# Kernel tuning notes

Hardware: AMD Instinct MI355X
Metric: run time of the kernel (lower is better)

## Reference

```python
import jax, jax.numpy as jnp
import numpy as np

B, T, S = 16, 512, 512
V, E, H = 10000, 512, 1024
L, K, MAXLEN = 6, 3, 1024
PAD_VAL = 1.0  # torch code pads conv input with tgt_pad_idx as a float value


def setup_inputs() -> dict:
    key = jax.random.key(0)
    ks = jax.random.split(key, 12)
    g = lambda k, shape: (jax.random.normal(k, shape, jnp.float32) * 0.02)
    return {
        "tgt": jax.random.randint(ks[0], (B, T), 0, V),
        "encoder_conved": jax.random.normal(ks[1], (B, S, E), jnp.float32),
        "encoder_combined": jax.random.normal(ks[2], (B, S, E), jnp.float32),
        "tok_emb": g(ks[3], (V, E)),
        "pos_emb": g(ks[4], (MAXLEN, E)),
        "emb2hid_w": g(ks[5], (E, H)), "emb2hid_b": jnp.zeros((H,), jnp.float32),
        "hid2emb_w": g(ks[6], (H, E)), "hid2emb_b": jnp.zeros((E,), jnp.float32),
        "attn_hid2emb_w": g(ks[7], (H, E)), "attn_hid2emb_b": jnp.zeros((E,), jnp.float32),
        "attn_emb2hid_w": g(ks[8], (E, H)), "attn_emb2hid_b": jnp.zeros((H,), jnp.float32),
        "fc_out_w": g(ks[9], (E, V)), "fc_out_b": jnp.zeros((V,), jnp.float32),
        "conv_w": g(ks[10], (L, 2 * H, H, K)),  # torch Conv1d weight: [out, in, k]
        "conv_b": jnp.zeros((L, 2 * H), jnp.float32),
    }


def reference(tgt, encoder_conved, encoder_combined, tok_emb, pos_emb,
              emb2hid_w, emb2hid_b, hid2emb_w, hid2emb_b,
              attn_hid2emb_w, attn_hid2emb_b, attn_emb2hid_w, attn_emb2hid_b,
              fc_out_w, fc_out_b, conv_w, conv_b):
    scale = jnp.float32(np.sqrt(0.5))
    b, t = tgt.shape
    h = emb2hid_w.shape[1]
    k = conv_w.shape[-1]

    # embeddings (dropout=0 -> identity)
    embedded = tok_emb[tgt] + pos_emb[jnp.arange(t)][None, :, :]   # [B,T,E]
    conv_input = (embedded @ emb2hid_w + emb2hid_b).transpose(0, 2, 1)  # [B,H,T]

    attention = None
    for l in range(conv_w.shape[0]):
        # causal left-pad with the (float) pad-index value, as in the torch code
        pad = jnp.full((b, h, k - 1), PAD_VAL, conv_input.dtype)
        x = jnp.concatenate([pad, conv_input], axis=2)              # [B,H,T+K-1]
        conved = jax.lax.conv_general_dilated(
            x, conv_w[l], window_strides=(1,), padding='VALID',
            dimension_numbers=('NCH', 'OIH', 'NCH')) + conv_b[l][None, :, None]  # [B,2H,T]
        a, g = jnp.split(conved, 2, axis=1)
        conved = a * jax.nn.sigmoid(g)                              # GLU -> [B,H,T]

        # single-head attention over encoder states
        conved_emb = conved.transpose(0, 2, 1) @ attn_hid2emb_w + attn_hid2emb_b  # [B,T,E]
        combined = (conved_emb + embedded) * scale
        energy = jnp.einsum('bte,bse->bts', combined, encoder_conved)
        attention = jax.nn.softmax(energy, axis=2)                  # [B,T,S]
        attended = jnp.einsum('bts,bse->bte', attention, encoder_combined)
        attended = attended @ attn_emb2hid_w + attn_emb2hid_b       # [B,T,H]
        conved = (conved + attended.transpose(0, 2, 1)) * scale     # [B,H,T]

        conv_input = (conved + conv_input) * scale                  # scaled residual

    conved = conv_input.transpose(0, 2, 1) @ hid2emb_w + hid2emb_b  # [B,T,E]
    output = conved @ fc_out_w + fc_out_b                           # [B,T,V]
    return output, attention
```

## Files before the change

### kernel.cpp

```cpp
#include <hip/hip_runtime.h>
#include <hip/hip_bf16.h>

typedef __attribute__((ext_vector_type(4))) float f32x4;
typedef __attribute__((ext_vector_type(8))) short short8;

#define DEVFN __device__ __forceinline__

static constexpr int Bn = 16, Tn = 512, Sn = 512, Vn = 10000, En = 512, Hn = 1024, Ln = 6;
static constexpr int Mn = Bn * Tn;
static constexpr float kScale = 0.70710678118654752440f;

DEVFN float bf2f(__hip_bfloat16 x) { return __bfloat162float(x); }
DEVFN __hip_bfloat16 f2bf(float x) { return __float2bfloat16(x); }

struct bf16x4 { __hip_bfloat16 x, y, z, w; };

DEVFN void gload_lds16(const short* g, short* l) {
    __builtin_amdgcn_global_load_lds((const __attribute__((address_space(1))) void*)g,
                                     (__attribute__((address_space(3))) void*)l, 16, 0, 0);
}


__global__ void padfill_kernel(__hip_bfloat16* p) {
    p[threadIdx.x] = f2bf(1.0f);
}

__global__ void embed_kernel(const int* __restrict__ tgt, const float* __restrict__ tok,
                             const float* __restrict__ pos, const float* __restrict__ bah,
                             __hip_bfloat16* __restrict__ out, __hip_bfloat16* __restrict__ outA) {
    int row = blockIdx.x;
    int t = row & (Tn - 1);
    int v = tgt[row];
    const float* tr = tok + (long)v * En;
    const float* pr = pos + (long)t * En;
    int e = threadIdx.x * 4;
    float4 a = *(const float4*)(tr + e);
    float4 b = *(const float4*)(pr + e);
    float4 bb = *(const float4*)(bah + e);
    bf16x4 o{f2bf(a.x + b.x), f2bf(a.y + b.y), f2bf(a.z + b.z), f2bf(a.w + b.w)};
    *(bf16x4*)(out + (long)row * En + e) = o;
    bf16x4 oa{f2bf(kScale * (a.x + b.x + bb.x)), f2bf(kScale * (a.y + b.y + bb.y)),
              f2bf(kScale * (a.z + b.z + bb.z)), f2bf(kScale * (a.w + b.w + bb.w))};
    *(bf16x4*)(outA + (long)row * En + e) = oa;
}

__global__ void transpose_f32_bf16(const float* __restrict__ src, __hip_bfloat16* __restrict__ dst,
                                   int R, int C, long sZi, long sZo) {
    __shared__ float tile[32][33];
    src += (long)blockIdx.z * sZi;
    dst += (long)blockIdx.z * sZo;
    int c0 = blockIdx.x * 32, r0 = blockIdx.y * 32;
    for (int i = threadIdx.y; i < 32; i += 8) {
        int r = r0 + i, c = c0 + threadIdx.x;
        tile[i][threadIdx.x] = (r < R && c < C) ? src[(long)r * C + c] : 0.f;
    }
    __syncthreads();
    for (int i = threadIdx.y; i < 32; i += 8) {
        int c = c0 + i, r = r0 + threadIdx.x;
        if (c < C && r < R) dst[(long)c * R + r] = f2bf(tile[threadIdx.x][i]);
    }
}

__global__ void convert_bf16_kernel(const float* __restrict__ src, __hip_bfloat16* __restrict__ dst,
                                    long n4) {
    long i = (long)blockIdx.x * blockDim.x + threadIdx.x;
    if (i >= n4) return;
    long j = i * 4;
    float4 v = *(const float4*)(src + j);
    bf16x4 o{f2bf(v.x), f2bf(v.y), f2bf(v.z), f2bf(v.w)};
    *(bf16x4*)(dst + j) = o;
}

__global__ __launch_bounds__(256) void wpack2_kernel(const float* __restrict__ convw,
                                                     __hip_bfloat16* __restrict__ wp, int l) {
    __shared__ float row[3 * Hn];
    int c = blockIdx.x;
    int grp = c >> 5, w = c & 31;
    int o = (w < 16) ? grp * 16 + w : Hn + grp * 16 + (w - 16);
    const float* src = convw + ((long)(l * 2 * Hn + o)) * (Hn * 3);
#pragma unroll
    for (int j = 0; j < 3; ++j) {
        int idx = (j * 256 + threadIdx.x) * 4;
        *(float4*)&row[idx] = *(const float4*)(src + idx);
    }
    __syncthreads();
    __hip_bfloat16* dst = wp + (long)c * (3 * Hn);
#pragma unroll
    for (int j = 0; j < 3; ++j) {
        int kk = (j * 256 + threadIdx.x) * 4;
        int tap = kk >> 10;
        int i = kk & (Hn - 1);
        bf16x4 v{f2bf(row[i * 3 + tap]), f2bf(row[(i + 1) * 3 + tap]),
                 f2bf(row[(i + 2) * 3 + tap]), f2bf(row[(i + 3) * 3 + tap])};
        *(bf16x4*)(dst + kk) = v;
    }
}

__global__ __launch_bounds__(256) void softmax_kernel(const float* __restrict__ energy,
                                                      float* __restrict__ attn_f32,
                                                      __hip_bfloat16* __restrict__ attn_bf) {
    int row = blockIdx.x;
    const float* e = energy + (long)row * Sn;
    int tid = threadIdx.x;
    float v0 = e[tid], v1 = e[tid + 256];
    float m = fmaxf(v0, v1);
    for (int off = 32; off; off >>= 1) m = fmaxf(m, __shfl_xor(m, off));
    __shared__ float redm[4];
    __shared__ float reds[4];
    int lane = tid & 63, w = tid >> 6;
    if (lane == 0) redm[w] = m;
    __syncthreads();
    m = fmaxf(fmaxf(redm[0], redm[1]), fmaxf(redm[2], redm[3]));
    float x0 = __expf(v0 - m), x1 = __expf(v1 - m);
    float s = x0 + x1;
    for (int off = 32; off; off >>= 1) s += __shfl_xor(s, off);
    if (lane == 0) reds[w] = s;
    __syncthreads();
    s = reds[0] + reds[1] + reds[2] + reds[3];
    float inv = 1.f / s;
    long base = (long)row * Sn;
    if (attn_f32) {
        attn_f32[base + tid] = x0 * inv;
        attn_f32[base + tid + 256] = x1 * inv;
    }
    attn_bf[base + tid] = f2bf(x0 * inv);
    attn_bf[base + tid + 256] = f2bf(x1 * inv);
}

template <int EPI, bool OUTF32, bool NBOUND>
__global__ __launch_bounds__(256) void gemm_bf16(
    const __hip_bfloat16* __restrict__ A, const __hip_bfloat16* __restrict__ Bw,
    const float* __restrict__ bias, void* __restrict__ Cout,
    const __hip_bfloat16* __restrict__ R1, const __hip_bfloat16* __restrict__ R2,
    const float* __restrict__ R1f, const __hip_bfloat16* __restrict__ padrow,
    int M, int N, int K, long aZ, long bZ, long cZ, float s1, float s2) {
    __shared__ alignas(16) short As[2][128 * 32];
    __shared__ alignas(16) short Bs[2][128 * 32];
    const int tid = threadIdx.x;
    const int lane = tid & 63;
    const int wid = tid >> 6;
    const int wr = wid >> 1, wc = wid & 1;
    const int m0 = blockIdx.y * 128, n0 = blockIdx.x * 128;
    const short* Ag = (const short*)A + (long)blockIdx.z * aZ;
    const short* Bg = (const short*)Bw + (long)blockIdx.z * bZ;
    const short* pad = (const short*)padrow;

    f32x4 acc[4][4] = {};

    const int rc = tid >> 2;
    const int k8 = (tid & 3) * 8;

    auto stage = [&](int buf, int k0) {
#pragma unroll
        for (int j = 0; j < 2; ++j) {
            int r = rc + j * 64;
            const short* asrc = Ag + (long)(m0 + r) * K + k0 + k8;
            gload_lds16(asrc, &As[buf][r * 32 + k8]);
            int n = n0 + r;
            const short* bsrc = (NBOUND && n >= N) ? (pad + k8) : (Bg + (long)n * K + k0 + k8);
            gload_lds16(bsrc, &Bs[buf][r * 32 + k8]);
        }
    };

    stage(0, 0);
    __syncthreads();

    int cur = 0;
    for (int k0 = 0; k0 < K; k0 += 32) {
        if (k0 + 32 < K) stage(cur ^ 1, k0 + 32);
        const int rsel = lane & 15, hi = (lane >> 4) * 8;
        short8 af[4], bg[4];
#pragma unroll
        for (int mi = 0; mi < 4; ++mi)
            af[mi] = *(const short8*)&As[cur][(wr * 64 + mi * 16 + rsel) * 32 + hi];
#pragma unroll
        for (int ni = 0; ni < 4; ++ni)
            bg[ni] = *(const short8*)&Bs[cur][(wc * 64 + ni * 16 + rsel) * 32 + hi];
#pragma unroll
        for (int mi = 0; mi < 4; ++mi)
#pragma unroll
            for (int ni = 0; ni < 4; ++ni)
                acc[mi][ni] = __builtin_amdgcn_mfma_f32_16x16x32_bf16(af[mi], bg[ni], acc[mi][ni], 0, 0, 0);
        __syncthreads();
        cur ^= 1;
    }

    const int rsel = lane & 15, rg = (lane >> 4) * 4;
    float* Cf = (float*)Cout + (long)blockIdx.z * cZ;
    __hip_bfloat16* Cb = (__hip_bfloat16*)Cout + (long)blockIdx.z * cZ;
    const __hip_bfloat16* R1z = R1 + (long)blockIdx.z * cZ;
    const __hip_bfloat16* R2z = R2 + (long)blockIdx.z * cZ;
    const float* R1fz = R1f + (long)blockIdx.z * cZ;
#pragma unroll
    for (int ni = 0; ni < 4; ++ni) {
        int col = n0 + wc * 64 + ni * 16 + rsel;
        if (NBOUND && col >= N) continue;
        float bi = (EPI != 3 && bias) ? bias[col] : 0.f;
#pragma unroll
        for (int mi = 0; mi < 4; ++mi) {
            int row = m0 + wr * 64 + mi * 16 + rg;
            f32x4 v = acc[mi][ni];
#pragma unroll
            for (int q = 0; q < 4; ++q) {
                long idx = (long)(row + q) * N + col;
                float x;
                if (EPI == 3) x = v[q] * s1 + R1fz[idx];
                else {
                    x = v[q] + bi;
                    if (EPI >= 1) x = (x + bf2f(R1z[idx])) * s1;
                    if (EPI >= 2) x = (x + bf2f(R2z[idx])) * s2;
                }
                if (OUTF32) Cf[idx] = x;
                else Cb[idx] = f2bf(x);
            }
        }
    }
}

template <bool OUTF32, bool GLUE, bool IM2COL, bool NBOUND>
__global__ __launch_bounds__(512, 2) void gemm256(
    const __hip_bfloat16* __restrict__ A, const __hip_bfloat16* __restrict__ Bw,
    const float* __restrict__ bias, void* __restrict__ Cout,
    const __hip_bfloat16* __restrict__ padrow, int M, int N, int K) {
    __shared__ alignas(16) short As[2][256 * 64];
    __shared__ alignas(16) short Bs[2][256 * 64];
    const int tid = threadIdx.x;
    const int lane = tid & 63;
    const int wid = tid >> 6;
    const int wr = wid >> 2, wc = wid & 3;
    const int nwg = gridDim.x * gridDim.y;
    const int orig = blockIdx.y * gridDim.x + blockIdx.x;
    const int qd = nwg >> 3, rd = nwg & 7, xc = orig & 7, loc = orig >> 3;
    const int bid = (xc < rd ? xc * (qd + 1) : rd * (qd + 1) + (xc - rd) * qd) + loc;
    const int n0 = (bid % gridDim.x) * 256, m0 = (bid / gridDim.x) * 256;
    const short* Ag = (const short*)A;
    const short* Bg = (const short*)Bw;
    const short* pad = (const short*)padrow;

    f32x4 acc[8][4] = {};

    const int srow_l = tid >> 3;
    const int scol = ((tid & 7) ^ (srow_l & 7)) * 8;
    const int sdst = (tid >> 3) * 64 + (tid & 7) * 8;

    auto stage = [&](int buf, int kt) {
        const int k0 = kt * 64;
#pragma unroll
        for (int j = 0; j < 4; ++j) {
            const int row = j * 64 + srow_l;
            const short* asrc;
            if (IM2COL) {
                int m = m0 + row;
                int t = m & (Tn - 1);
                int tap = k0 >> 10;
                int tau = t - 2 + tap;
                int kcol = (k0 & (Hn - 1)) + scol;
                asrc = (tau >= 0) ? (Ag + (long)(m - 2 + tap) * Hn + kcol) : (pad + scol);
            } else {
                asrc = Ag + (long)(m0 + row) * K + k0 + scol;
            }
            gload_lds16(asrc, &As[buf][j * 4096 + sdst]);
            int n = n0 + row;
            const short* bsrc = (NBOUND && n >= N) ? (pad + scol) : (Bg + (long)n * K + k0 + scol);
            gload_lds16(bsrc, &Bs[buf][j * 4096 + sdst]);
        }
    };

    const int rsel = lane & 15, hi = (lane >> 4) * 8;
    const int xorc = (rsel & 7) << 3;

    stage(0, 0);
    const int NT = K >> 6;
    for (int t = 0; t < NT; ++t) {
        const int cur = t & 1;
        if (t + 1 < NT) {
            stage(cur ^ 1, t + 1);
            asm volatile("s_waitcnt vmcnt(8)" ::: "memory");
        } else {
            asm volatile("s_waitcnt vmcnt(0)" ::: "memory");
        }
        __builtin_amdgcn_s_barrier();
        __builtin_amdgcn_sched_barrier(0);
        short8 bg[2][2][2];
#pragma unroll
        for (int nh = 0; nh < 2; ++nh)
#pragma unroll
            for (int i = 0; i < 2; ++i) {
                const int row = wc * 64 + nh * 32 + i * 16 + rsel;
#pragma unroll
                for (int ks = 0; ks < 2; ++ks)
                    bg[nh][i][ks] = *(const short8*)&Bs[cur][row * 64 + ((ks * 32 + hi) ^ xorc)];
            }
#pragma unroll
        for (int mh = 0; mh < 2; ++mh) {
            short8 af[4][2];
#pragma unroll
            for (int i = 0; i < 4; ++i) {
                const int row = wr * 128 + mh * 64 + i * 16 + rsel;
#pragma unroll
                for (int ks = 0; ks < 2; ++ks)
                    af[i][ks] = *(const short8*)&As[cur][row * 64 + ((ks * 32 + hi) ^ xorc)];
            }
            __builtin_amdgcn_s_setprio(1);
#pragma unroll
            for (int nh = 0; nh < 2; ++nh)
#pragma unroll
                for (int i = 0; i < 4; ++i)
#pragma unroll
                    for (int jn = 0; jn < 2; ++jn)
#pragma unroll
                        for (int ks = 0; ks < 2; ++ks)
                            acc[mh * 4 + i][nh * 2 + jn] = __builtin_amdgcn_mfma_f32_16x16x32_bf16(
                                af[i][ks], bg[nh][jn][ks], acc[mh * 4 + i][nh * 2 + jn], 0, 0, 0);
            __builtin_amdgcn_s_setprio(0);
            __builtin_amdgcn_sched_barrier(0);
        }
        __builtin_amdgcn_s_barrier();
        __builtin_amdgcn_sched_barrier(0);
    }

    const int rg = (lane >> 4) * 4;
    if (GLUE) {
        __hip_bfloat16* Cb = (__hip_bfloat16*)Cout;
        const int No = N >> 1;
#pragma unroll
        for (int p = 0; p < 2; ++p) {
            int jcol = ((n0 + wc * 64) >> 1) + p * 16 + rsel;
            float ba = bias[jcol];
            float bgv = bias[Hn + jcol];
#pragma unroll
            for (int mi = 0; mi < 8; ++mi) {
                int row = m0 + wr * 128 + mi * 16 + rg;
                f32x4 va = acc[mi][2 * p], vg = acc[mi][2 * p + 1];
#pragma unroll
                for (int q = 0; q < 4; ++q) {
                    float a = va[q] + ba;
                    float g = vg[q] + bgv;
                    Cb[(long)(row + q) * No + jcol] = f2bf(a * (1.f / (1.f + __expf(-g))));
                }
            }
        }
        return;
    }
    float* Cf = (float*)Cout;
    __hip_bfloat16* Cb = (__hip_bfloat16*)Cout;
#pragma unroll
    for (int ni = 0; ni < 4; ++ni) {
        int col = n0 + wc * 64 + ni * 16 + rsel;
        if (NBOUND && col >= N) continue;
        float bi = bias ? bias[col] : 0.f;
#pragma unroll
        for (int mi = 0; mi < 8; ++mi) {
            int row = m0 + wr * 128 + mi * 16 + rg;
            f32x4 v = acc[mi][ni];
#pragma unroll
            for (int q = 0; q < 4; ++q) {
                long idx = (long)(row + q) * N + col;
                float x = v[q] + bi;
                if (OUTF32) Cf[idx] = x;
                else Cb[idx] = f2bf(x);
            }
        }
    }
}


extern "C" void kernel_launch(void* const* d_in, const int* in_sizes, int n_in,
                              void* d_out, int out_size, void* d_ws, size_t ws_size,
                              hipStream_t stream) {
    const int* tgt = (const int*)d_in[0];
    const float* enc_conved = (const float*)d_in[1];
    const float* enc_combined = (const float*)d_in[2];
    const float* tok_emb = (const float*)d_in[3];
    const float* pos_emb = (const float*)d_in[4];
    const float* w_e2h = (const float*)d_in[5];
    const float* b_e2h = (const float*)d_in[6];
    const float* w_h2e = (const float*)d_in[7];
    const float* b_h2e = (const float*)d_in[8];
    const float* w_ah2e = (const float*)d_in[9];
    const float* b_ah2e = (const float*)d_in[10];
    const float* w_ae2h = (const float*)d_in[11];
    const float* b_ae2h = (const float*)d_in[12];
    const float* w_fc = (const float*)d_in[13];
    const float* b_fc = (const float*)d_in[14];
    const float* conv_w = (const float*)d_in[15];
    const float* conv_b = (const float*)d_in[16];

    char* ws = (char*)d_ws;
    size_t off = 0;
    auto alloc = [&](size_t bytes) { size_t r = off; off = (off + bytes + 255) & ~(size_t)255; return r; };
    __hip_bfloat16* emb    = (__hip_bfloat16*)(ws + alloc((size_t)Mn * En * 2));
    __hip_bfloat16* embA   = (__hip_bfloat16*)(ws + alloc((size_t)Mn * En * 2));
    __hip_bfloat16* convin = (__hip_bfloat16*)(ws + alloc((size_t)Mn * Hn * 2));
    __hip_bfloat16* conved = (__hip_bfloat16*)(ws + alloc((size_t)Mn * Hn * 2));
    size_t o_en = alloc((size_t)Mn * Sn * 4);
    float* energy = (float*)(ws + o_en);
    __hip_bfloat16* encm = (__hip_bfloat16*)(ws + o_en);
    __hip_bfloat16* attnbf = (__hip_bfloat16*)(ws + alloc((size_t)Mn * Sn * 2));
    __hip_bfloat16* wT_e2h = (__hip_bfloat16*)(ws + alloc((size_t)Hn * En * 2));
    __hip_bfloat16* wT_h2e = (__hip_bfloat16*)(ws + alloc((size_t)En * Hn * 2));
    __hip_bfloat16* wT_ae2h= (__hip_bfloat16*)(ws + alloc((size_t)Hn * En * 2));
    __hip_bfloat16* wbAH   = (__hip_bfloat16*)(ws + alloc((size_t)Hn * En * 2));
    __hip_bfloat16* wT_fc  = (__hip_bfloat16*)(ws + alloc((size_t)Vn * En * 2));
    __hip_bfloat16* encc   = (__hip_bfloat16*)(ws + alloc((size_t)Bn * Sn * En * 2));
    __hip_bfloat16* encAH  = (__hip_bfloat16*)(ws + alloc((size_t)Bn * Sn * Hn * 2));
    __hip_bfloat16* encCW  = (__hip_bfloat16*)(ws + alloc((size_t)Bn * Hn * Sn * 2));
    float* embE            = (float*)(ws + alloc((size_t)Mn * Sn * 4));
    __hip_bfloat16* padrow = (__hip_bfloat16*)(ws + alloc(256));
    __hip_bfloat16* wpack  = (__hip_bfloat16*)(ws + alloc((size_t)2 * Hn * 3 * Hn * 2));
    __hip_bfloat16* tmpE = conved;

    float* out = (float*)d_out;
    float* attn_out = out + (long)Mn * Vn;
    const long bSq = (long)Sn * Sn;
    const long bSH = (long)Sn * Hn;

    dim3 tb(32, 8);
    const __hip_bfloat16* nb = nullptr;
    const float* nf = nullptr;

    padfill_kernel<<<1, 128, 0, stream>>>(padrow);
    embed_kernel<<<Mn, 128, 0, stream>>>(tgt, tok_emb, pos_emb, b_ah2e, emb, embA);
    transpose_f32_bf16<<<dim3(Hn / 32, En / 32, 1), tb, 0, stream>>>(w_e2h, wT_e2h, En, Hn, 0, 0);
    transpose_f32_bf16<<<dim3(En / 32, Hn / 32, 1), tb, 0, stream>>>(w_h2e, wT_h2e, Hn, En, 0, 0);
    transpose_f32_bf16<<<dim3(Hn / 32, En / 32, 1), tb, 0, stream>>>(w_ae2h, wT_ae2h, En, Hn, 0, 0);
    transpose_f32_bf16<<<dim3((Vn + 31) / 32, En / 32, 1), tb, 0, stream>>>(w_fc, wT_fc, En, Vn, 0, 0);
    convert_bf16_kernel<<<((long)Hn * En / 4 + 255) / 256, 256, 0, stream>>>(w_ah2e, wbAH, (long)Hn * En / 4);
    convert_bf16_kernel<<<((long)Bn * Sn * En / 4 + 255) / 256, 256, 0, stream>>>(enc_conved, encc, (long)Bn * Sn * En / 4);
    convert_bf16_kernel<<<((long)Bn * Sn * En / 4 + 255) / 256, 256, 0, stream>>>(enc_combined, encm, (long)Bn * Sn * En / 4);

    gemm_bf16<0, false, false><<<dim3(Hn / 128, Sn / 128, Bn), 256, 0, stream>>>(
        encc, wbAH, nullptr, encAH, nb, nb, nf, padrow, Sn, Hn, En, bSq, 0, bSH, 1.f, 1.f);
    gemm_bf16<0, false, false><<<dim3(Sn / 128, Hn / 128, Bn), 256, 0, stream>>>(
        wT_ae2h, encm, nullptr, encCW, nb, nb, nf, padrow, Hn, Sn, En, 0, bSq, bSH, 1.f, 1.f);
    gemm_bf16<0, true, false><<<dim3(Sn / 128, Tn / 128, Bn), 256, 0, stream>>>(
        embA, encc, nullptr, embE, nb, nb, nf, padrow, Tn, Sn, En, bSq, bSq, bSq, 1.f, 1.f);
    gemm_bf16<0, false, false><<<dim3(Hn / 128, Mn / 128, 1), 256, 0, stream>>>(
        emb, wT_e2h, b_e2h, convin, nb, nb, nf, padrow, Mn, Hn, En, 0, 0, 0, 1.f, 1.f);

    for (int l = 0; l < Ln; ++l) {
        wpack2_kernel<<<2 * Hn, 256, 0, stream>>>(conv_w, wpack, l);
        gemm256<false, true, true, false><<<dim3(2 * Hn / 256, Mn / 256, 1), 512, 0, stream>>>(
            convin, wpack, conv_b + (long)l * 2 * Hn, conved, padrow, Mn, 2 * Hn, 3 * Hn);
        gemm_bf16<3, true, false><<<dim3(Sn / 128, Tn / 128, Bn), 256, 0, stream>>>(
            conved, encAH, nullptr, energy, nb, nb, embE, padrow,
            Tn, Sn, Hn, (long)Tn * Hn, bSH, bSq, kScale, 1.f);
        softmax_kernel<<<Mn, 256, 0, stream>>>(energy, (l == Ln - 1) ? attn_out : nullptr, attnbf);
        gemm_bf16<2, false, false><<<dim3(Hn / 128, Tn / 128, Bn), 256, 0, stream>>>(
            attnbf, encCW, b_ae2h, convin, conved, convin, nf, padrow,
            Tn, Hn, Sn, bSq, bSH, (long)Tn * Hn, kScale, kScale);
    }

    gemm_bf16<0, false, false><<<dim3(En / 128, Mn / 128, 1), 256, 0, stream>>>(
        convin, wT_h2e, b_h2e, tmpE, nb, nb, nf, padrow, Mn, En, Hn, 0, 0, 0, 1.f, 1.f);
    gemm256<true, false, false, true><<<dim3((Vn + 255) / 256, Mn / 256, 1), 512, 0, stream>>>(
        tmpE, wT_fc, b_fc, out, padrow, Mn, Vn, En);
}
```

Before: 1.321 ms.

## Split tile prefetch into quarters interleaved with four MFMA quadrant phases

The GEMM main loop now runs four compute phases, one per 128x128 quadrant of the 256x256 tile. Each phase issues a quarter of the next k-tile's global-to-LDS loads, separated by barriers, instead of issuing the whole prefetch up front. The aim is to spread memory traffic across the MFMA work and cut fragment register pressure by loading B halves separately. The cost is three more workgroup barriers per k-iteration, plus tighter waitcnt reasoning that has to stay correct for the double buffer.

```diff
diff --git a/kernel.cpp b/kernel.cpp
--- a/kernel.cpp
+++ b/kernel.cpp
@@ -243,10 +243,10 @@
     const int scol = ((tid & 7) ^ (srow_l & 7)) * 8;
     const int sdst = (tid >> 3) * 64 + (tid & 7) * 8;
 
-    auto stage = [&](int buf, int kt) {
+    auto stageA = [&](int buf, int kt, int half) {
         const int k0 = kt * 64;
 #pragma unroll
-        for (int j = 0; j < 4; ++j) {
+        for (int j = half * 2; j < half * 2 + 2; ++j) {
             const int row = j * 64 + srow_l;
             const short* asrc;
             if (IM2COL) {
@@ -260,6 +260,13 @@
                 asrc = Ag + (long)(m0 + row) * K + k0 + scol;
             }
             gload_lds16(asrc, &As[buf][j * 4096 + sdst]);
+        }
+    };
+    auto stageB = [&](int buf, int kt, int half) {
+        const int k0 = kt * 64;
+#pragma unroll
+        for (int j = half * 2; j < half * 2 + 2; ++j) {
+            const int row = j * 64 + srow_l;
             int n = n0 + row;
             const short* bsrc = (NBOUND && n >= N) ? (pad + scol) : (Bg + (long)n * K + k0 + scol);
             gload_lds16(bsrc, &Bs[buf][j * 4096 + sdst]);
@@ -269,52 +276,99 @@
     const int rsel = lane & 15, hi = (lane >> 4) * 8;
     const int xorc = (rsel & 7) << 3;
 
-    stage(0, 0);
+    stageA(0, 0, 0); stageA(0, 0, 1); stageB(0, 0, 0); stageB(0, 0, 1);
+
     const int NT = K >> 6;
     for (int t = 0; t < NT; ++t) {
         const int cur = t & 1;
-        if (t + 1 < NT) {
-            stage(cur ^ 1, t + 1);
-            asm volatile("s_waitcnt vmcnt(8)" ::: "memory");
+        const int nxt = cur ^ 1;
+        const bool pf = (t + 1 < NT);
+        short8 af[4][2], bg0[2][2], bg1[2][2];
+
+        if (pf) {
+            stageA(nxt, t + 1, 0);
+            asm volatile("s_waitcnt vmcnt(2)" ::: "memory");
         } else {
             asm volatile("s_waitcnt vmcnt(0)" ::: "memory");
         }
         __builtin_amdgcn_s_barrier();
         __builtin_amdgcn_sched_barrier(0);
-        short8 bg[2][2][2];
-#pragma unroll
-        for (int nh = 0; nh < 2; ++nh)
-#pragma unroll
-            for (int i = 0; i < 2; ++i) {
-                const int row = wc * 64 + nh * 32 + i * 16 + rsel;
+#pragma unroll
+        for (int i = 0; i < 4; ++i) {
+            const int row = wr * 128 + 0 * 64 + i * 16 + rsel;
+#pragma unroll
+            for (int ks = 0; ks < 2; ++ks)
+                af[i][ks] = *(const short8*)&As[cur][row * 64 + ((ks * 32 + hi) ^ xorc)];
+        }
+#pragma unroll
+        for (int i = 0; i < 2; ++i) {
+            const int row = wc * 64 + 0 * 32 + i * 16 + rsel;
+#pragma unroll
+            for (int ks = 0; ks < 2; ++ks)
+                bg0[i][ks] = *(const short8*)&Bs[cur][row * 64 + ((ks * 32 + hi) ^ xorc)];
+        }
+        __builtin_amdgcn_s_setprio(1);
+#pragma unroll
+        for (int i = 0; i < 4; ++i)
+#pragma unroll
+            for (int jn = 0; jn < 2; ++jn)
 #pragma unroll
                 for (int ks = 0; ks < 2; ++ks)
-                    bg[nh][i][ks] = *(const short8*)&Bs[cur][row * 64 + ((ks * 32 + hi) ^ xorc)];
-            }
-#pragma unroll
-        for (int mh = 0; mh < 2; ++mh) {
-            short8 af[4][2];
-#pragma unroll
-            for (int i = 0; i < 4; ++i) {
-                const int row = wr * 128 + mh * 64 + i * 16 + rsel;
+                    acc[i][jn] = __builtin_amdgcn_mfma_f32_16x16x32_bf16(af[i][ks], bg0[jn][ks], acc[i][jn], 0, 0, 0);
+        __builtin_amdgcn_s_setprio(0);
+        __builtin_amdgcn_s_barrier();
+        __builtin_amdgcn_sched_barrier(0);
+
+        if (pf) stageA(nxt, t + 1, 1);
+#pragma unroll
+        for (int i = 0; i < 2; ++i) {
+            const int row = wc * 64 + 1 * 32 + i * 16 + rsel;
+#pragma unroll
+            for (int ks = 0; ks < 2; ++ks)
+                bg1[i][ks] = *(const short8*)&Bs[cur][row * 64 + ((ks * 32 + hi) ^ xorc)];
+        }
+        __builtin_amdgcn_s_setprio(1);
+#pragma unroll
+        for (int i = 0; i < 4; ++i)
+#pragma unroll
+            for (int jn = 0; jn < 2; ++jn)
 #pragma unroll
                 for (int ks = 0; ks < 2; ++ks)
-                    af[i][ks] = *(const short8*)&As[cur][row * 64 + ((ks * 32 + hi) ^ xorc)];
-            }
-            __builtin_amdgcn_s_setprio(1);
-#pragma unroll
-            for (int nh = 0; nh < 2; ++nh)
-#pragma unroll
-                for (int i = 0; i < 4; ++i)
-#pragma unroll
-                    for (int jn = 0; jn < 2; ++jn)
-#pragma unroll
-                        for (int ks = 0; ks < 2; ++ks)
-                            acc[mh * 4 + i][nh * 2 + jn] = __builtin_amdgcn_mfma_f32_16x16x32_bf16(
-                                af[i][ks], bg[nh][jn][ks], acc[mh * 4 + i][nh * 2 + jn], 0, 0, 0);
-            __builtin_amdgcn_s_setprio(0);
-            __builtin_amdgcn_sched_barrier(0);
-        }
+                    acc[i][2 + jn] = __builtin_amdgcn_mfma_f32_16x16x32_bf16(af[i][ks], bg1[jn][ks], acc[i][2 + jn], 0, 0, 0);
+        __builtin_amdgcn_s_setprio(0);
+        __builtin_amdgcn_s_barrier();
+        __builtin_amdgcn_sched_barrier(0);
+
+        if (pf) stageB(nxt, t + 1, 0);
+#pragma unroll
+        for (int i = 0; i < 4; ++i) {
+            const int row = wr * 128 + 1 * 64 + i * 16 + rsel;
+#pragma unroll
+            for (int ks = 0; ks < 2; ++ks)
+                af[i][ks] = *(const short8*)&As[cur][row * 64 + ((ks * 32 + hi) ^ xorc)];
+        }
+        __builtin_amdgcn_s_setprio(1);
+#pragma unroll
+        for (int i = 0; i < 4; ++i)
+#pragma unroll
+            for (int jn = 0; jn < 2; ++jn)
+#pragma unroll
+                for (int ks = 0; ks < 2; ++ks)
+                    acc[4 + i][jn] = __builtin_amdgcn_mfma_f32_16x16x32_bf16(af[i][ks], bg0[jn][ks], acc[4 + i][jn], 0, 0, 0);
+        __builtin_amdgcn_s_setprio(0);
+        __builtin_amdgcn_s_barrier();
+        __builtin_amdgcn_sched_barrier(0);
+
+        if (pf) stageB(nxt, t + 1, 1);
+        __builtin_amdgcn_s_setprio(1);
+#pragma unroll
+        for (int i = 0; i < 4; ++i)
+#pragma unroll
+            for (int jn = 0; jn < 2; ++jn)
+#pragma unroll
+                for (int ks = 0; ks < 2; ++ks)
+                    acc[4 + i][2 + jn] = __builtin_amdgcn_mfma_f32_16x16x32_bf16(af[i][ks], bg1[jn][ks], acc[4 + i][2 + jn], 0, 0, 0);
+        __builtin_amdgcn_s_setprio(0);
         __builtin_amdgcn_s_barrier();
         __builtin_amdgcn_sched_barrier(0);
     }
```

After: 1.453 ms. 1.1x slower.

## Pad conv input per batch and reuse one A tile across all three taps

Applied to the files above, without the earlier changes.

The hidden-state buffer now lives in a per-batch padded layout: each sequence is preceded by two rows filled with the pad value. A new dedicated conv+GLU kernel loads one 384-row A tile per K-step from this layout. It reads all three causal taps out of that tile by shifting the row offset, instead of reloading A through an im2col address computation per tap. Downstream GEMMs are re-batched with new strides and a separate residual stride so they address the padded buffer. The trade-offs are a larger LDS footprint (about 147 KB, one block per CU), extra unused rows staged per tile, and hand-tuned waitcnt and barrier scheduling.

```diff
diff --git a/kernel.cpp b/kernel.cpp
--- a/kernel.cpp
+++ b/kernel.cpp
@@ -8,6 +8,7 @@
 
 static constexpr int Bn = 16, Tn = 512, Sn = 512, Vn = 10000, En = 512, Hn = 1024, Ln = 6;
 static constexpr int Mn = Bn * Tn;
+static constexpr int TP = Tn + 2;
 static constexpr float kScale = 0.70710678118654752440f;
 
 DEVFN float bf2f(__hip_bfloat16 x) { return __bfloat162float(x); }
@@ -23,6 +24,14 @@
 
 __global__ void padfill_kernel(__hip_bfloat16* p) {
     p[threadIdx.x] = f2bf(1.0f);
+}
+
+__global__ void padrows_kernel(__hip_bfloat16* convinP) {
+    int row = blockIdx.x;
+    long base = ((long)(row >> 1) * TP + (row & 1)) * Hn;
+    int e = threadIdx.x * 4;
+    bf16x4 v{f2bf(1.f), f2bf(1.f), f2bf(1.f), f2bf(1.f)};
+    *(bf16x4*)(convinP + base + e) = v;
 }
 
 __global__ void embed_kernel(const int* __restrict__ tgt, const float* __restrict__ tok,
@@ -133,7 +142,7 @@
     const float* __restrict__ bias, void* __restrict__ Cout,
     const __hip_bfloat16* __restrict__ R1, const __hip_bfloat16* __restrict__ R2,
     const float* __restrict__ R1f, const __hip_bfloat16* __restrict__ padrow,
-    int M, int N, int K, long aZ, long bZ, long cZ, float s1, float s2) {
+    int M, int N, int K, long aZ, long bZ, long cZ, long r1Z, float s1, float s2) {
     __shared__ alignas(16) short As[2][128 * 32];
     __shared__ alignas(16) short Bs[2][128 * 32];
     const int tid = threadIdx.x;
@@ -188,9 +197,9 @@
     const int rsel = lane & 15, rg = (lane >> 4) * 4;
     float* Cf = (float*)Cout + (long)blockIdx.z * cZ;
     __hip_bfloat16* Cb = (__hip_bfloat16*)Cout + (long)blockIdx.z * cZ;
-    const __hip_bfloat16* R1z = R1 + (long)blockIdx.z * cZ;
+    const __hip_bfloat16* R1z = R1 + (long)blockIdx.z * r1Z;
     const __hip_bfloat16* R2z = R2 + (long)blockIdx.z * cZ;
-    const float* R1fz = R1f + (long)blockIdx.z * cZ;
+    const float* R1fz = R1f + (long)blockIdx.z * r1Z;
 #pragma unroll
     for (int ni = 0; ni < 4; ++ni) {
         int col = n0 + wc * 64 + ni * 16 + rsel;
@@ -217,8 +226,124 @@
     }
 }
 
-template <bool OUTF32, bool GLUE, bool IM2COL, bool NBOUND>
-__global__ __launch_bounds__(512, 2) void gemm256(
+__global__ __launch_bounds__(512) void conv_glu_kernel(
+    const __hip_bfloat16* __restrict__ Ain,
+    const __hip_bfloat16* __restrict__ Bw,
+    const float* __restrict__ bias, __hip_bfloat16* __restrict__ Cout,
+    const __hip_bfloat16* __restrict__ padrow) {
+    __shared__ alignas(16) short As[2][384 * 32];
+    __shared__ alignas(16) short Bs[2][3 * 256 * 32];
+    const int tid = threadIdx.x;
+    const int lane = tid & 63;
+    const int wid = tid >> 6;
+    const int wr = wid >> 2, wc = wid & 3;
+    const int nwg = gridDim.x * gridDim.y;
+    const int orig = blockIdx.y * gridDim.x + blockIdx.x;
+    const int qd = nwg >> 3, rd = nwg & 7, xc = orig & 7, loc = orig >> 3;
+    const int bid = (xc < rd ? xc * (qd + 1) : rd * (qd + 1) + (xc - rd) * qd) + loc;
+    const int n0 = (bid % gridDim.x) * 256, m0 = (bid / gridDim.x) * 256;
+    const short* Ag = (const short*)Ain;
+    const short* Bg = (const short*)Bw;
+    const short* pad = (const short*)padrow;
+    const int p0 = (m0 >> 9) * TP + 2 + (m0 & 511);
+
+    f32x4 acc[8][4] = {};
+
+    const int srow = tid >> 2;
+    const int skey = (tid >> 3) & 3;
+    const int scol = ((tid & 3) ^ skey) * 8;
+    const int sdst = tid * 8;
+
+    auto stageA = [&](int buf, int kt) {
+        const int k0 = kt * 32;
+#pragma unroll
+        for (int j = 0; j < 3; ++j) {
+            int prow = p0 - 128 + j * 128 + srow;
+            const short* src = (prow >= 0) ? (Ag + (long)prow * Hn + k0 + scol) : (pad + scol);
+            gload_lds16(src, &As[buf][j * 4096 + sdst]);
+        }
+    };
+    auto stageB = [&](int buf, int kt) {
+        const int k0 = kt * 32;
+#pragma unroll
+        for (int tap = 0; tap < 3; ++tap)
+#pragma unroll
+            for (int j = 0; j < 2; ++j) {
+                int row = j * 128 + srow;
+                const short* src = Bg + (long)(n0 + row) * 3072 + tap * 1024 + k0 + scol;
+                gload_lds16(src, &Bs[buf][tap * 8192 + j * 4096 + sdst]);
+            }
+    };
+
+    const int rsel = lane & 15, hi = (lane >> 4) * 8;
+
+    stageA(0, 0); stageB(0, 0);
+    for (int t = 0; t < 32; ++t) {
+        const int cur = t & 1;
+        if (t + 1 < 32) {
+            stageA(cur ^ 1, t + 1); stageB(cur ^ 1, t + 1);
+            asm volatile("s_waitcnt vmcnt(9)" ::: "memory");
+        } else {
+            asm volatile("s_waitcnt vmcnt(0)" ::: "memory");
+        }
+        __builtin_amdgcn_s_barrier();
+        __builtin_amdgcn_sched_barrier(0);
+#pragma unroll
+        for (int tap = 0; tap < 3; ++tap) {
+            short8 bg[4];
+#pragma unroll
+            for (int ni = 0; ni < 4; ++ni) {
+                int row = wc * 64 + ni * 16 + rsel;
+                int xk = ((row >> 1) & 3) << 3;
+                bg[ni] = *(const short8*)&Bs[cur][tap * 8192 + row * 32 + (hi ^ xk)];
+            }
+#pragma unroll
+            for (int mh = 0; mh < 2; ++mh) {
+                short8 af[4];
+#pragma unroll
+                for (int i = 0; i < 4; ++i) {
+                    int row = 126 + tap + wr * 128 + mh * 64 + i * 16 + rsel;
+                    int xk = ((row >> 1) & 3) << 3;
+                    af[i] = *(const short8*)&As[cur][row * 32 + (hi ^ xk)];
+                }
+                __builtin_amdgcn_s_setprio(1);
+#pragma unroll
+                for (int i = 0; i < 4; ++i)
+#pragma unroll
+                    for (int ni = 0; ni < 4; ++ni)
+                        acc[mh * 4 + i][ni] = __builtin_amdgcn_mfma_f32_16x16x32_bf16(
+                            af[i], bg[ni], acc[mh * 4 + i][ni], 0, 0, 0);
+                __builtin_amdgcn_s_setprio(0);
+                __builtin_amdgcn_sched_barrier(0);
+            }
+        }
+        __builtin_amdgcn_s_barrier();
+        __builtin_amdgcn_sched_barrier(0);
+    }
+
+    const int rg = (lane >> 4) * 4;
+    const int No = Hn;
+#pragma unroll
+    for (int p = 0; p < 2; ++p) {
+        int jcol = ((n0 + wc * 64) >> 1) + p * 16 + rsel;
+        float ba = bias[jcol];
+        float bgv = bias[Hn + jcol];
+#pragma unroll
+        for (int mi = 0; mi < 8; ++mi) {
+            int row = m0 + wr * 128 + mi * 16 + rg;
+            f32x4 va = acc[mi][2 * p], vg = acc[mi][2 * p + 1];
+#pragma unroll
+            for (int q = 0; q < 4; ++q) {
+                float a = va[q] + ba;
+                float g = vg[q] + bgv;
+                Cout[(long)(row + q) * No + jcol] = f2bf(a * (1.f / (1.f + __expf(-g))));
+            }
+        }
+    }
+}
+
+template <bool OUTF32, bool NBOUND>
+__global__ __launch_bounds__(512) void gemm256(
     const __hip_bfloat16* __restrict__ A, const __hip_bfloat16* __restrict__ Bw,
     const float* __restrict__ bias, void* __restrict__ Cout,
     const __hip_bfloat16* __restrict__ padrow, int M, int N, int K) {
@@ -248,17 +373,7 @@
 #pragma unroll
         for (int j = 0; j < 4; ++j) {
             const int row = j * 64 + srow_l;
-            const short* asrc;
-            if (IM2COL) {
-                int m = m0 + row;
-                int t = m & (Tn - 1);
-                int tap = k0 >> 10;
-                int tau = t - 2 + tap;
-                int kcol = (k0 & (Hn - 1)) + scol;
-                asrc = (tau >= 0) ? (Ag + (long)(m - 2 + tap) * Hn + kcol) : (pad + scol);
-            } else {
-                asrc = Ag + (long)(m0 + row) * K + k0 + scol;
-            }
+            const short* asrc = Ag + (long)(m0 + row) * K + k0 + scol;
             gload_lds16(asrc, &As[buf][j * 4096 + sdst]);
             int n = n0 + row;
             const short* bsrc = (NBOUND && n >= N) ? (pad + scol) : (Bg + (long)n * K + k0 + scol);
@@ -320,28 +435,6 @@
     }
 
     const int rg = (lane >> 4) * 4;
-    if (GLUE) {
-        __hip_bfloat16* Cb = (__hip_bfloat16*)Cout;
-        const int No = N >> 1;
-#pragma unroll
-        for (int p = 0; p < 2; ++p) {
-            int jcol = ((n0 + wc * 64) >> 1) + p * 16 + rsel;
-            float ba = bias[jcol];
-            float bgv = bias[Hn + jcol];
-#pragma unroll
-            for (int mi = 0; mi < 8; ++mi) {
-                int row = m0 + wr * 128 + mi * 16 + rg;
-                f32x4 va = acc[mi][2 * p], vg = acc[mi][2 * p + 1];
-#pragma unroll
-                for (int q = 0; q < 4; ++q) {
-                    float a = va[q] + ba;
-                    float g = vg[q] + bgv;
-                    Cb[(long)(row + q) * No + jcol] = f2bf(a * (1.f / (1.f + __expf(-g))));
-                }
-            }
-        }
-        return;
-    }
     float* Cf = (float*)Cout;
     __hip_bfloat16* Cb = (__hip_bfloat16*)Cout;
 #pragma unroll
@@ -391,7 +484,7 @@
     auto alloc = [&](size_t bytes) { size_t r = off; off = (off + bytes + 255) & ~(size_t)255; return r; };
     __hip_bfloat16* emb    = (__hip_bfloat16*)(ws + alloc((size_t)Mn * En * 2));
     __hip_bfloat16* embA   = (__hip_bfloat16*)(ws + alloc((size_t)Mn * En * 2));
-    __hip_bfloat16* convin = (__hip_bfloat16*)(ws + alloc((size_t)Mn * Hn * 2));
+    __hip_bfloat16* convinP= (__hip_bfloat16*)(ws + alloc((size_t)Bn * TP * Hn * 2));
     __hip_bfloat16* conved = (__hip_bfloat16*)(ws + alloc((size_t)Mn * Hn * 2));
     size_t o_en = alloc((size_t)Mn * Sn * 4);
     float* energy = (float*)(ws + o_en);
@@ -409,17 +502,21 @@
     __hip_bfloat16* padrow = (__hip_bfloat16*)(ws + alloc(256));
     __hip_bfloat16* wpack  = (__hip_bfloat16*)(ws + alloc((size_t)2 * Hn * 3 * Hn * 2));
     __hip_bfloat16* tmpE = conved;
+    __hip_bfloat16* convinD = convinP + 2 * Hn;
 
     float* out = (float*)d_out;
     float* attn_out = out + (long)Mn * Vn;
     const long bSq = (long)Sn * Sn;
     const long bSH = (long)Sn * Hn;
+    const long bTH = (long)Tn * Hn;
+    const long bPH = (long)TP * Hn;
 
     dim3 tb(32, 8);
     const __hip_bfloat16* nb = nullptr;
     const float* nf = nullptr;
 
     padfill_kernel<<<1, 128, 0, stream>>>(padrow);
+    padrows_kernel<<<2 * Bn, 256, 0, stream>>>(convinP);
     embed_kernel<<<Mn, 128, 0, stream>>>(tgt, tok_emb, pos_emb, b_ah2e, emb, embA);
     transpose_f32_bf16<<<dim3(Hn / 32, En / 32, 1), tb, 0, stream>>>(w_e2h, wT_e2h, En, Hn, 0, 0);
     transpose_f32_bf16<<<dim3(En / 32, Hn / 32, 1), tb, 0, stream>>>(w_h2e, wT_h2e, Hn, En, 0, 0);
@@ -430,29 +527,29 @@
     convert_bf16_kernel<<<((long)Bn * Sn * En / 4 + 255) / 256, 256, 0, stream>>>(enc_combined, encm, (long)Bn * Sn * En / 4);
 
     gemm_bf16<0, false, false><<<dim3(Hn / 128, Sn / 128, Bn), 256, 0, stream>>>(
-        encc, wbAH, nullptr, encAH, nb, nb, nf, padrow, Sn, Hn, En, bSq, 0, bSH, 1.f, 1.f);
+        encc, wbAH, nullptr, encAH, nb, nb, nf, padrow, Sn, Hn, En, bSq, 0, bSH, 0, 1.f, 1.f);
     gemm_bf16<0, false, false><<<dim3(Sn / 128, Hn / 128, Bn), 256, 0, stream>>>(
-        wT_ae2h, encm, nullptr, encCW, nb, nb, nf, padrow, Hn, Sn, En, 0, bSq, bSH, 1.f, 1.f);
+        wT_ae2h, encm, nullptr, encCW, nb, nb, nf, padrow, Hn, Sn, En, 0, bSq, bSH, 0, 1.f, 1.f);
     gemm_bf16<0, true, false><<<dim3(Sn / 128, Tn / 128, Bn), 256, 0, stream>>>(
-        embA, encc, nullptr, embE, nb, nb, nf, padrow, Tn, Sn, En, bSq, bSq, bSq, 1.f, 1.f);
-    gemm_bf16<0, false, false><<<dim3(Hn / 128, Mn / 128, 1), 256, 0, stream>>>(
-        emb, wT_e2h, b_e2h, convin, nb, nb, nf, padrow, Mn, Hn, En, 0, 0, 0, 1.f, 1.f);
+        embA, encc, nullptr, embE, nb, nb, nf, padrow, Tn, Sn, En, bSq, bSq, bSq, 0, 1.f, 1.f);
+    gemm_bf16<0, false, false><<<dim3(Hn / 128, Tn / 128, Bn), 256, 0, stream>>>(
+        emb, wT_e2h, b_e2h, convinD, nb, nb, nf, padrow, Tn, Hn, En, (long)Tn * En, 0, bPH, 0, 1.f, 1.f);
 
     for (int l = 0; l < Ln; ++l) {
         wpack2_kernel<<<2 * Hn, 256, 0, stream>>>(conv_w, wpack, l);
-        gemm256<false, true, true, false><<<dim3(2 * Hn / 256, Mn / 256, 1), 512, 0, stream>>>(
-            convin, wpack, conv_b + (long)l * 2 * Hn, conved, padrow, Mn, 2 * Hn, 3 * Hn);
+        conv_glu_kernel<<<dim3(2 * Hn / 256, Mn / 256), 512, 0, stream>>>(
+            convinP, wpack, conv_b + (long)l * 2 * Hn, conved, padrow);
         gemm_bf16<3, true, false><<<dim3(Sn / 128, Tn / 128, Bn), 256, 0, stream>>>(
             conved, encAH, nullptr, energy, nb, nb, embE, padrow,
-            Tn, Sn, Hn, (long)Tn * Hn, bSH, bSq, kScale, 1.f);
+            Tn, Sn, Hn, bTH, bSH, bSq, bSq, kScale, 1.f);
         softmax_kernel<<<Mn, 256, 0, stream>>>(energy, (l == Ln - 1) ? attn_out : nullptr, attnbf);
         gemm_bf16<2, false, false><<<dim3(Hn / 128, Tn / 128, Bn), 256, 0, stream>>>(
-            attnbf, encCW, b_ae2h, convin, conved, convin, nf, padrow,
-            Tn, Hn, Sn, bSq, bSH, (long)Tn * Hn, kScale, kScale);
-    }
-
-    gemm_bf16<0, false, false><<<dim3(En / 128, Mn / 128, 1), 256, 0, stream>>>(
-        convin, wT_h2e, b_h2e, tmpE, nb, nb, nf, padrow, Mn, En, Hn, 0, 0, 0, 1.f, 1.f);
-    gemm256<true, false, false, true><<<dim3((Vn + 255) / 256, Mn / 256, 1), 512, 0, stream>>>(
+            attnbf, encCW, b_ae2h, convinD, conved, convinD, nf, padrow,
+            Tn, Hn, Sn, bSq, bSH, bPH, bTH, kScale, kScale);
+    }
+
+    gemm_bf16<0, false, false><<<dim3(En / 128, Tn / 128, Bn), 256, 0, stream>>>(
+        convinD, wT_h2e, b_h2e, tmpE, nb, nb, nf, padrow, Tn, En, Hn, bPH, 0, (long)Tn * En, 0, 1.f, 1.f);
+    gemm256<true, true><<<dim3((Vn + 255) / 256, Mn / 256), 512, 0, stream>>>(
         tmpE, wT_fc, b_fc, out, padrow, Mn, Vn, En);
 }
```

Result: no change. 1.303 ms (-1.4%).
